# Kernel tuning notes

Hardware: AMD Instinct MI355X
Metric: run time of the kernel (lower is better)

Reference implementation:

```python
import jax, jax.numpy as jnp
from jax import lax
import numpy as np

B, T, H, V, C = 64, 64, 1024, 32000, 10
Z, CD = 32, 8  # latent dim, cond embedding dim


def lstm_scan(x_tbh, h0, c0, Wih, Whh, bih, bhh):
    """PyTorch-convention LSTM over time. x_tbh: [T,B,H]; returns hs [T,B,H]."""
    def step(carry, x):
        h, c = carry
        gates = x @ Wih.T + bih + h @ Whh.T + bhh  # [B,4H]
        i, f, g, o = jnp.split(gates, 4, axis=-1)
        c = jax.nn.sigmoid(f) * c + jax.nn.sigmoid(i) * jnp.tanh(g)
        h = jax.nn.sigmoid(o) * jnp.tanh(c)
        return (h, c), h
    _, hs = lax.scan(step, (h0, c0), x_tbh)
    return hs


def setup_inputs() -> dict:
    key = jax.random.key(0)
    ks = jax.random.split(key, 24)
    s = 0.02
    d = {
        'input_word': jax.random.randint(ks[0], (B, T), 0, V),
        'cond': jax.random.randint(ks[1], (B,), 0, C),
        'emb_N': jax.random.normal(ks[2], (V, H), jnp.float32) * s,
        'Wih_N': jax.random.normal(ks[3], (4 * H, H), jnp.float32) * s,
        'Whh_N': jax.random.normal(ks[4], (4 * H, H), jnp.float32) * s,
        'bih_N': jnp.zeros((4 * H,), jnp.float32),
        'bhh_N': jnp.zeros((4 * H,), jnp.float32),
        'emb_D': jax.random.normal(ks[5], (V, H), jnp.float32) * s,
        'Wih_D': jax.random.normal(ks[6], (4 * H, H), jnp.float32) * s,
        'Whh_D': jax.random.normal(ks[7], (4 * H, H), jnp.float32) * s,
        'bih_D': jnp.zeros((4 * H,), jnp.float32),
        'bhh_D': jnp.zeros((4 * H,), jnp.float32),
        'emb_cond': jax.random.normal(ks[8], (C, CD), jnp.float32) * s,
        'W_mean': jax.random.normal(ks[9], (Z, H), jnp.float32) * s,
        'b_mean': jnp.zeros((Z,), jnp.float32),
        'W_logvar': jax.random.normal(ks[10], (Z, H), jnp.float32) * s,
        'b_logvar': jnp.zeros((Z,), jnp.float32),
        'W_st': jax.random.normal(ks[11], (H, Z + CD), jnp.float32) * s,
        'b_st': jnp.zeros((H,), jnp.float32),
        'W_out': jax.random.normal(ks[12], (V, H), jnp.float32) * s,
        'b_out': jnp.zeros((V,), jnp.float32),
        'eps': jax.random.normal(ks[13], (B, Z), jnp.float32),
    }
    return d


def reference(input_word, cond, emb_N, Wih_N, Whh_N, bih_N, bhh_N,
              emb_D, Wih_D, Whh_D, bih_D, bhh_D, emb_cond,
              W_mean, b_mean, W_logvar, b_logvar, W_st, b_st,
              W_out, b_out, eps):
    cond_e = emb_cond[cond]                              # [B,8]
    # ---- encoder ----
    x_enc = jnp.transpose(emb_N[input_word], (1, 0, 2))  # [T,B,H]
    h0 = jnp.concatenate([jnp.zeros((B, H - CD), x_enc.dtype), cond_e], axis=-1)
    c0 = jnp.zeros((B, H), x_enc.dtype)
    hs = lstm_scan(x_enc, h0, c0, Wih_N, Whh_N, bih_N, bhh_N)
    h_t = hs[-1]                                         # [B,H]
    mean_h = h_t @ W_mean.T + b_mean                     # [B,32]
    logvar_h = h_t @ W_logvar.T + b_logvar               # [B,32]
    latent_h = eps * jnp.exp(0.5 * logvar_h) + mean_h    # reparameterize
    # ---- decoder (teacher forcing, start token 0) ----
    hd0 = jnp.concatenate([latent_h, cond_e], axis=-1) @ W_st.T + b_st  # [B,H]
    cd0 = jnp.zeros((B, H), hd0.dtype)
    dec_tok = jnp.concatenate(
        [jnp.zeros((B, 1), input_word.dtype), input_word[:, :-1]], axis=1)
    x_dec = jnp.transpose(emb_D[dec_tok], (1, 0, 2))     # [T,B,H]
    hs_d = lstm_scan(x_dec, hd0, cd0, Wih_D, Whh_D, bih_D, bhh_D)  # [T,B,H]
    logits = hs_d @ W_out.T + b_out                      # [T,B,V]
    return jnp.transpose(logits, (1, 0, 2))              # [B,T,V]
```

## Files before the change

kernel.cpp:

```cpp
#include <hip/hip_runtime.h>
#include <hip/hip_bf16.h>

typedef unsigned short u16;
typedef unsigned int   u32;
typedef unsigned long long u64;
typedef __attribute__((ext_vector_type(8))) short short8;
typedef __attribute__((ext_vector_type(4))) float f32x4;

#define DEVINL static __device__ __forceinline__

DEVINL u16 f2bf(float x) {
  u32 u = __float_as_uint(x);
  u32 r = (u + 0x7fffu + ((u >> 16) & 1u)) >> 16;
  return (u16)r;
}

#define GLD16(gp, lp) __builtin_amdgcn_global_load_lds(                     \
    (const __attribute__((address_space(1))) u32*)(gp),                     \
    (__attribute__((address_space(3))) u32*)(lp), 16, 0, 0)

__global__ __launch_bounds__(256) void conv_all(
    const float* __restrict__ s0, u16* __restrict__ d0,
    const float* __restrict__ s1, u16* __restrict__ d1,
    const float* __restrict__ s2, u16* __restrict__ d2,
    const float* __restrict__ s3, u16* __restrict__ d3,
    const float* __restrict__ s4, u16* __restrict__ d4) {
  const float* s; u16* d; int local;
  int blk = blockIdx.x;
  if (blk < 16384) {
    int p = blk >> 12; local = blk & 4095;
    s = (p == 0) ? s0 : (p == 1) ? s1 : (p == 2) ? s2 : s3;
    d = (p == 0) ? d0 : (p == 1) ? d1 : (p == 2) ? d2 : d3;
  } else {
    s = s4; d = d4; local = blk - 16384;
  }
  int i = local * 256 + threadIdx.x;
  float4 v = ((const float4*)s)[i];
  ushort4 o;
  o.x = f2bf(v.x); o.y = f2bf(v.y); o.z = f2bf(v.z); o.w = f2bf(v.w);
  ((ushort4*)d)[i] = o;
}

__global__ __launch_bounds__(256) void prep_small(
    const int* __restrict__ cond, const float* __restrict__ emb_cond,
    const float* __restrict__ bihN, const float* __restrict__ bhhN,
    const float* __restrict__ bihD, const float* __restrict__ bhhD,
    float* __restrict__ ce, float* __restrict__ biasN, float* __restrict__ biasD,
    u32* __restrict__ bar) {
  int tid = blockIdx.x * 256 + threadIdx.x;
  if (tid < 512) {
    int b = tid >> 3, j = tid & 7;
    ce[tid] = emb_cond[cond[b] * 8 + j];
  }
  int i = tid - 512;
  if (i >= 0 && i < 4096) {
    biasN[i] = bihN[i] + bhhN[i];
    biasD[i] = bihD[i] + bhhD[i];
  }
  int k = tid - 4608;
  if (k >= 0 && k < 512) bar[k] = 0;
}

__global__ __launch_bounds__(256) void init_enc(const float* __restrict__ ce,
                                                u16* __restrict__ hb0) {
  int tid = blockIdx.x * 256 + threadIdx.x;
  int b = tid >> 10, col = tid & 1023;
  float v = (col >= 1016) ? ce[b * 8 + (col - 1016)] : 0.f;
  hb0[tid] = f2bf(v);
}

__global__ __launch_bounds__(256) void gather_kernel(const float* __restrict__ emb,
                                                     const int* __restrict__ words,
                                                     u16* __restrict__ X, int dec) {
  int r = blockIdx.x;
  int t = r >> 6, b = r & 63;
  int tok = dec ? ((t == 0) ? 0 : words[b * 64 + t - 1]) : words[b * 64 + t];
  float4 v = ((const float4*)(emb + (size_t)tok * 1024))[threadIdx.x];
  ushort4 o;
  o.x = f2bf(v.x); o.y = f2bf(v.y); o.z = f2bf(v.z); o.w = f2bf(v.w);
  ((ushort4*)(X + (size_t)r * 1024))[threadIdx.x] = o;
}

DEVINL void gemm0_body(char* smemc, int bid, int nwg,
                       const u16* __restrict__ A, const u16* __restrict__ B,
                       float* __restrict__ C, const float* __restrict__ bias,
                       int N, int K) {
  u16 (*lA)[256 * 32] = (u16(*)[256 * 32])smemc;
  u16 (*lB)[128 * 32] = (u16(*)[128 * 32])(smemc + 32768);
  const int tid = threadIdx.x;
  const int lane = tid & 63;
  const int wid = tid >> 6;

  const int nn = N >> 7;
  const int wgid = (bid & 7) * (nwg >> 3) + (bid >> 3);
  const int tile_m = (wgid / nn) * 256;
  const int tile_n = (wgid % nn) * 128;
  const int wm = wid >> 1, wn = wid & 1;

  const int ldr = lane >> 2;
  const int lko = (lane & 3) * 8;
  const int l15 = lane & 15;
  const int g4 = lane >> 4;

  const size_t aBase = (size_t)tile_m * K;
  const size_t bBase = (size_t)tile_n * K;

  auto stage = [&](int buf, int k0) {
#pragma unroll
    for (int q = 0; q < 2; ++q) {
      int chk = wid * 2 + q;
      int row = chk * 16 + ldr;
      GLD16(A + aBase + (size_t)row * K + k0 + lko, &lA[buf][chk * 512]);
    }
    int row = wid * 16 + ldr;
    GLD16(B + bBase + (size_t)row * K + k0 + lko, &lB[buf][wid * 512]);
  };

  f32x4 acc[4][4];
#pragma unroll
  for (int i = 0; i < 4; ++i)
#pragma unroll
    for (int j = 0; j < 4; ++j) acc[i][j] = (f32x4)0.f;

  stage(0, 0);
  __syncthreads();

  const int NIT = K >> 5;
  for (int it = 0; it < NIT; ++it) {
    const int cur = it & 1;
    if (it + 1 < NIT) stage(cur ^ 1, (it + 1) * 32);
    short8 af[4], bf[4];
#pragma unroll
    for (int i = 0; i < 4; ++i)
      af[i] = *(const short8*)&lA[cur][(wm * 64 + i * 16 + l15) * 32 + g4 * 8];
#pragma unroll
    for (int j = 0; j < 4; ++j)
      bf[j] = *(const short8*)&lB[cur][(wn * 64 + j * 16 + l15) * 32 + g4 * 8];
#pragma unroll
    for (int i = 0; i < 4; ++i)
#pragma unroll
      for (int j = 0; j < 4; ++j)
        acc[i][j] = __builtin_amdgcn_mfma_f32_16x16x32_bf16(af[i], bf[j], acc[i][j], 0, 0, 0);
    __syncthreads();
  }

#pragma unroll
  for (int i = 0; i < 4; ++i) {
    int row0 = tile_m + wm * 64 + i * 16 + (g4 << 2);
#pragma unroll
    for (int j = 0; j < 4; ++j) {
      int col = tile_n + wn * 64 + j * 16 + l15;
      float bv = bias[col];
#pragma unroll
      for (int e = 0; e < 4; ++e)
        C[(size_t)(row0 + e) * (size_t)N + col] = acc[i][j][e] + bv;
    }
  }
}

DEVINL void lstm_body(char* smemc, const u16* __restrict__ Whh,
                      const float* __restrict__ Xp, u16* __restrict__ hbuf,
                      u16* __restrict__ hs_out, float* __restrict__ hT_out,
                      u32* arrive, int wgi) {
  char* smemA = smemc;
  float (*lg)[16][16] = (float(*)[16][16])(smemc + 32768);
  const int tid = threadIdx.x;
  const int lane = tid & 63;
  const int v = tid >> 6;
  const int gate = v >> 1;
  const int ch = v & 1;
  const int c = wgi >> 5;
  const int j = wgi & 31;
  const int b0 = c * 16, col0 = j * 32;
  const int l15 = lane & 15, g4 = lane >> 4;

  short8 breg[32];
  {
    const u16* Brow = Whh + (size_t)(gate * 1024 + col0 + ch * 16 + l15) * 1024
                          + g4 * 8;
#pragma unroll
    for (int kk = 0; kk < 32; ++kk)
      breg[kk] = *(const short8*)(Brow + kk * 32);
  }

  const int crow = tid >> 5, colw = tid & 31;
  const int bg = b0 + crow, cgl = col0 + colw;
  const int ch2 = colw >> 4, cw = colw & 15;
  float creg = 0.f;

  float xg0, xg1, xg2, xg3;
  {
    size_t xrow = (size_t)bg * 4096 + cgl;
    xg0 = __builtin_nontemporal_load(&Xp[xrow]);
    xg1 = __builtin_nontemporal_load(&Xp[xrow + 1024]);
    xg2 = __builtin_nontemporal_load(&Xp[xrow + 2048]);
    xg3 = __builtin_nontemporal_load(&Xp[xrow + 3072]);
  }

  for (int t = 0; t < 64; ++t) {
    const char* rbase = (const char*)(hbuf + (size_t)(t & 1) * 65536)
                      + (size_t)b0 * 2048;
    u32* wb32 = (u32*)(hbuf + (size_t)((t + 1) & 1) * 65536);

#pragma unroll
    for (int q = 0; q < 4; ++q) {
      int g = q * 512 + tid;
      int row = g >> 7;
      int cb = (g & 127) * 16;
      const u64* src = (const u64*)(rbase + (size_t)row * 2048 + cb);
      u64 lo = __hip_atomic_load(src,     __ATOMIC_RELAXED, __HIP_MEMORY_SCOPE_AGENT);
      u64 hi = __hip_atomic_load(src + 1, __ATOMIC_RELAXED, __HIP_MEMORY_SCOPE_AGENT);
      u64* d = (u64*)(smemA + row * 2048 + (cb ^ ((row & 7) << 4)));
      d[0] = lo; d[1] = hi;
    }
    __syncthreads();

    f32x4 a4[4] = {(f32x4)0.f, (f32x4)0.f, (f32x4)0.f, (f32x4)0.f};
#pragma unroll
    for (int kk = 0; kk < 32; ++kk) {
      int cb2 = kk * 64 + g4 * 16;
      const short8 a = *(const short8*)(smemA + l15 * 2048 + (cb2 ^ ((l15 & 7) << 4)));
      a4[kk & 3] = __builtin_amdgcn_mfma_f32_16x16x32_bf16(a, breg[kk], a4[kk & 3], 0, 0, 0);
    }
    f32x4 asum = a4[0] + a4[1] + a4[2] + a4[3];
    {
      int m = g4 * 4;
#pragma unroll
      for (int e = 0; e < 4; ++e) lg[v][m + e][l15] = asum[e];
    }
    __syncthreads();

    {
      float gi = lg[0 + ch2][crow][cw] + xg0;
      float gf = lg[2 + ch2][crow][cw] + xg1;
      float gg = lg[4 + ch2][crow][cw] + xg2;
      float go = lg[6 + ch2][crow][cw] + xg3;
      float si = 1.f / (1.f + __expf(-gi));
      float sf = 1.f / (1.f + __expf(-gf));
      float so = 1.f / (1.f + __expf(-go));
      float tg = tanhf(gg);
      float cn = sf * creg + si * tg;
      float hn = so * tanhf(cn);
      creg = cn;
      u16 h16 = f2bf(hn);
      u32 mine = h16;
      u32 other = (u32)__shfl_xor((int)mine, 1);
      if (!(colw & 1)) {
        u32 pk = mine | (other << 16);
        __hip_atomic_store(wb32 + (((size_t)bg * 1024 + cgl) >> 1), pk,
                           __ATOMIC_RELAXED, __HIP_MEMORY_SCOPE_AGENT);
      }
      if (hs_out) hs_out[((size_t)bg * 64 + t) * 1024 + cgl] = h16;
      if (hT_out && t == 63) hT_out[bg * 1024 + cgl] = hn;
    }

    if (t != 63) {
      {
        size_t xrow = (size_t)((t + 1) * 64 + bg) * 4096 + cgl;
        xg0 = __builtin_nontemporal_load(&Xp[xrow]);
        xg1 = __builtin_nontemporal_load(&Xp[xrow + 1024]);
        xg2 = __builtin_nontemporal_load(&Xp[xrow + 2048]);
        xg3 = __builtin_nontemporal_load(&Xp[xrow + 3072]);
      }
      u32 want = (u32)(t + 1);
      asm volatile("s_waitcnt vmcnt(0)" ::: "memory");
      __syncthreads();
      if (tid == 0)
        __hip_atomic_store(&arrive[wgi], want, __ATOMIC_RELAXED,
                           __HIP_MEMORY_SCOPE_AGENT);
      if (tid < 32) {
        int guard = 0;
        while (__hip_atomic_load(&arrive[c * 32 + tid], __ATOMIC_RELAXED,
                                 __HIP_MEMORY_SCOPE_AGENT) < want) {
          __builtin_amdgcn_s_sleep(2);
          if (++guard > (1 << 20)) break;
        }
      }
      __syncthreads();
    }
  }
}

__global__ __launch_bounds__(512, 1) void lstm_cluster(
    const u16* __restrict__ Whh, const float* __restrict__ Xp,
    u16* __restrict__ hbuf, u16* __restrict__ hs_out,
    float* __restrict__ hT_out, u32* arrive) {
  __shared__ __align__(16) char smem[40960];
  lstm_body(smem, Whh, Xp, hbuf, hs_out, hT_out, arrive, blockIdx.x);
}

__global__ __launch_bounds__(512) void gemm_bt0(
    const u16* __restrict__ A, const u16* __restrict__ B,
    float* __restrict__ C, const float* __restrict__ bias, int N, int K) {
  __shared__ __align__(16) char smem[49152];
  gemm0_body(smem, blockIdx.x, gridDim.x, A, B, C, bias, N, K);
}

__global__ __launch_bounds__(512, 1) void enc_fused(
    const u16* __restrict__ whhN, const float* __restrict__ XpE,
    u16* __restrict__ hbuf, float* __restrict__ hT_out, u32* arrive,
    const u16* __restrict__ Xd, const u16* __restrict__ wihD,
    float* __restrict__ XpD, const float* __restrict__ biasD) {
  __shared__ __align__(16) char smem[49152];
  if (blockIdx.x < 128)
    lstm_body(smem, whhN, XpE, hbuf, nullptr, hT_out, arrive, blockIdx.x);
  else
    gemm0_body(smem, blockIdx.x - 128, 512, Xd, wihD, XpD, biasD, 4096, 1024);
}

__global__ __launch_bounds__(512) void gemm_bt1(
    const u16* __restrict__ A, const u16* __restrict__ B,
    float* __restrict__ C, const float* __restrict__ bias, int N, int K) {
  __shared__ u16 lA[2][256 * 32];
  __shared__ u16 lB[2][128 * 32];
  const int tid = threadIdx.x;
  const int lane = tid & 63;
  const int wid = tid >> 6;

  const int i = blockIdx.x;
  const int x = i & 7;
  const int k = i >> 3;
  const int mg = k >> 6;
  const int r  = k & 63;
  const int kn = r >> 1;
  const int mi = r & 1;
  const int tn = kn * 8 + x;
  if (tn >= 250) return;
  const int tile_m = (mg * 2 + mi) * 256;
  const int tile_n = tn * 128;
  const int wm = wid >> 1, wn = wid & 1;

  const int ldr = lane >> 2;
  const int lko = (lane & 3) * 8;
  const int l15 = lane & 15;
  const int g4 = lane >> 4;

  const size_t aBase = (size_t)tile_m * K;
  const size_t bBase = (size_t)tile_n * K;

  auto stage = [&](int buf, int k0) {
#pragma unroll
    for (int q = 0; q < 2; ++q) {
      int chk = wid * 2 + q;
      int row = chk * 16 + ldr;
      GLD16(A + aBase + (size_t)row * K + k0 + lko, &lA[buf][chk * 512]);
    }
    int row = wid * 16 + ldr;
    GLD16(B + bBase + (size_t)row * K + k0 + lko, &lB[buf][wid * 512]);
  };

  f32x4 acc[4][4];
#pragma unroll
  for (int i2 = 0; i2 < 4; ++i2)
#pragma unroll
    for (int j2 = 0; j2 < 4; ++j2) acc[i2][j2] = (f32x4)0.f;

  stage(0, 0);
  __syncthreads();

  const int NIT = K >> 5;
  for (int it = 0; it < NIT; ++it) {
    const int cur = it & 1;
    if (it + 1 < NIT) stage(cur ^ 1, (it + 1) * 32);
    short8 af[4], bf[4];
#pragma unroll
    for (int i2 = 0; i2 < 4; ++i2)
      af[i2] = *(const short8*)&lA[cur][(wm * 64 + i2 * 16 + l15) * 32 + g4 * 8];
#pragma unroll
    for (int j2 = 0; j2 < 4; ++j2)
      bf[j2] = *(const short8*)&lB[cur][(wn * 64 + j2 * 16 + l15) * 32 + g4 * 8];
#pragma unroll
    for (int i2 = 0; i2 < 4; ++i2)
#pragma unroll
      for (int j2 = 0; j2 < 4; ++j2)
        acc[i2][j2] = __builtin_amdgcn_mfma_f32_16x16x32_bf16(af[i2], bf[j2], acc[i2][j2], 0, 0, 0);
    __syncthreads();
  }

#pragma unroll
  for (int i2 = 0; i2 < 4; ++i2) {
    int row0 = tile_m + wm * 64 + i2 * 16 + (g4 << 2);
#pragma unroll
    for (int j2 = 0; j2 < 4; ++j2) {
      int col = tile_n + wn * 64 + j2 * 16 + l15;
      float bv = bias[col];
#pragma unroll
      for (int e = 0; e < 4; ++e) {
        size_t o = (size_t)(row0 + e) * (size_t)N + col;
        __builtin_nontemporal_store(acc[i2][j2][e] + bv, &C[o]);
      }
    }
  }
}

__global__ __launch_bounds__(256) void latent_hd0_kernel(
    const float* hT, const float* Wm, const float* bm,
    const float* Wl, const float* bl, const float* Wst, const float* bst,
    const float* eps, const float* ce, u16* hb0) {
  __shared__ float red[64][4];
  __shared__ float ml[64];
  __shared__ float lat[40];
  int b = blockIdx.x;
  int tid = threadIdx.x;
  int o = tid >> 2, p = tid & 3;
  const float* w = (o < 32) ? (Wm + (size_t)o * 1024) : (Wl + (size_t)(o - 32) * 1024);
  const float* h = hT + (size_t)b * 1024;
  float s = 0.f;
  for (int k = p * 256; k < p * 256 + 256; ++k) s += h[k] * w[k];
  red[o][p] = s;
  __syncthreads();
  if (tid < 64) {
    float v = red[tid][0] + red[tid][1] + red[tid][2] + red[tid][3];
    v += (tid < 32) ? bm[tid] : bl[tid - 32];
    ml[tid] = v;
  }
  __syncthreads();
  if (tid < 32) lat[tid] = eps[b * 32 + tid] * __expf(0.5f * ml[32 + tid]) + ml[tid];
  if (tid >= 32 && tid < 40) lat[tid] = ce[b * 8 + (tid - 32)];
  __syncthreads();
  for (int hc = tid; hc < 1024; hc += 256) {
    float s2 = bst[hc];
    const float* wr = Wst + (size_t)hc * 40;
#pragma unroll
    for (int j = 0; j < 40; ++j) s2 += lat[j] * wr[j];
    hb0[b * 1024 + hc] = f2bf(s2);
  }
}

extern "C" void kernel_launch(void* const* d_in, const int* in_sizes, int n_in,
                              void* d_out, int out_size, void* d_ws, size_t ws_size,
                              hipStream_t stream) {
  const int*   input_word = (const int*)d_in[0];
  const int*   cond       = (const int*)d_in[1];
  const float* emb_N      = (const float*)d_in[2];
  const float* Wih_N      = (const float*)d_in[3];
  const float* Whh_N      = (const float*)d_in[4];
  const float* bih_N      = (const float*)d_in[5];
  const float* bhh_N      = (const float*)d_in[6];
  const float* emb_D      = (const float*)d_in[7];
  const float* Wih_D      = (const float*)d_in[8];
  const float* Whh_D      = (const float*)d_in[9];
  const float* bih_D      = (const float*)d_in[10];
  const float* bhh_D      = (const float*)d_in[11];
  const float* emb_cond   = (const float*)d_in[12];
  const float* W_mean     = (const float*)d_in[13];
  const float* b_mean     = (const float*)d_in[14];
  const float* W_logvar   = (const float*)d_in[15];
  const float* b_logvar   = (const float*)d_in[16];
  const float* W_st       = (const float*)d_in[17];
  const float* b_st       = (const float*)d_in[18];
  const float* W_out      = (const float*)d_in[19];
  const float* b_out      = (const float*)d_in[20];
  const float* eps        = (const float*)d_in[21];
  float* out = (float*)d_out;

  char* ws = (char*)d_ws;
  size_t off = 0;
  auto alloc = [&](size_t b) { size_t p = off; off += (b + 255) & ~(size_t)255; return p; };
  u16*   wihN = (u16*)(ws + alloc(4096ull * 1024 * 2));
  u16*   whhN = (u16*)(ws + alloc(4096ull * 1024 * 2));
  u16*   wihD = (u16*)(ws + alloc(4096ull * 1024 * 2));
  u16*   whhD = (u16*)(ws + alloc(4096ull * 1024 * 2));
  u16*   wout = (u16*)(ws + alloc(32000ull * 1024 * 2));
  u16*   Xe   = (u16*)(ws + alloc(4096ull * 1024 * 2));
  u16*   Xd   = (u16*)(ws + alloc(4096ull * 1024 * 2));
  float* Xp   = (float*)(ws + alloc(4096ull * 4096 * 4));
  u16*   hsd  = (u16*)(ws + alloc(4096ull * 1024 * 2));
  u16*   hb   = (u16*)(ws + alloc(2ull * 64 * 1024 * 2));
  float* hf   = (float*)(ws + alloc(64ull * 1024 * 4));
  float* biasN = (float*)(ws + alloc(4096 * 4));
  float* biasD = (float*)(ws + alloc(4096 * 4));
  float* ce    = (float*)(ws + alloc(64 * 8 * 4));
  u32*   bar   = (u32*)(ws + alloc(2048));
  size_t base_off = off;
  float* XpD2 = (float*)(ws + alloc(4096ull * 4096 * 4));
  if (base_off > ws_size) return;
  const bool fused = (off <= ws_size);
  float* XpD = fused ? XpD2 : Xp;

  conv_all<<<48384, 256, 0, stream>>>(Wih_N, wihN, Whh_N, whhN,
                                      Wih_D, wihD, Whh_D, whhD, W_out, wout);
  prep_small<<<20, 256, 0, stream>>>(cond, emb_cond, bih_N, bhh_N, bih_D, bhh_D,
                                     ce, biasN, biasD, bar);
  gather_kernel<<<4096, 256, 0, stream>>>(emb_N, input_word, Xe, 0);
  gather_kernel<<<4096, 256, 0, stream>>>(emb_D, input_word, Xd, 1);
  init_enc<<<256, 256, 0, stream>>>(ce, hb);

  gemm_bt0<<<512, 512, 0, stream>>>(Xe, wihN, Xp, biasN, 4096, 1024);
  if (fused) {
    enc_fused<<<640, 512, 0, stream>>>(whhN, Xp, hb, hf, bar + 0,
                                       Xd, wihD, XpD, biasD);
  } else {
    lstm_cluster<<<128, 512, 0, stream>>>(whhN, Xp, hb, nullptr, hf, bar + 0);
  }
  latent_hd0_kernel<<<64, 256, 0, stream>>>(hf, W_mean, b_mean, W_logvar, b_logvar,
                                            W_st, b_st, eps, ce, hb);
  if (!fused)
    gemm_bt0<<<512, 512, 0, stream>>>(Xd, wihD, XpD, biasD, 4096, 1024);
  lstm_cluster<<<128, 512, 0, stream>>>(whhD, XpD, hb, hsd, nullptr, bar + 256);
  gemm_bt1<<<4096, 512, 0, stream>>>(hsd, wout, out, b_out, 32000, 1024);
}
```

Measured before the change: 1.011 ms.

## Overlap output projection with decoder LSTM and fold W_out conversion into encoder

Merges the decoder LSTM and the vocab projection GEMM into one launch. The LSTM blocks publish per-cluster progress counters, and the GEMM blocks spin on these counters until the timesteps their tile needs have been written, so the logits GEMM can start before the recurrence finishes. hs is now stored time-major and the output index is remapped to keep the [B,T,V] layout. The W_out fp32→bf16 conversion moves out of the upfront conversion kernel into spare blocks of the fused encoder launch, where it overlaps the serial encoder LSTM. This relies on GEMM blocks that spin while the LSTM blocks are co-resident and still able to make progress, and on inter-block flag ordering, so it risks deadlock or stale reads.

After: 998.2 us. About the same (-1.3%).

```diff
diff --git a/kernel.cpp b/kernel.cpp
--- a/kernel.cpp
+++ b/kernel.cpp
@@ -19,22 +19,25 @@
     (const __attribute__((address_space(1))) u32*)(gp),                     \
     (__attribute__((address_space(3))) u32*)(lp), 16, 0, 0)
 
-__global__ __launch_bounds__(256) void conv_all(
+__global__ __launch_bounds__(256) void conv4(
     const float* __restrict__ s0, u16* __restrict__ d0,
     const float* __restrict__ s1, u16* __restrict__ d1,
     const float* __restrict__ s2, u16* __restrict__ d2,
-    const float* __restrict__ s3, u16* __restrict__ d3,
-    const float* __restrict__ s4, u16* __restrict__ d4) {
-  const float* s; u16* d; int local;
+    const float* __restrict__ s3, u16* __restrict__ d3) {
   int blk = blockIdx.x;
-  if (blk < 16384) {
-    int p = blk >> 12; local = blk & 4095;
-    s = (p == 0) ? s0 : (p == 1) ? s1 : (p == 2) ? s2 : s3;
-    d = (p == 0) ? d0 : (p == 1) ? d1 : (p == 2) ? d2 : d3;
-  } else {
-    s = s4; d = d4; local = blk - 16384;
-  }
+  int p = blk >> 12, local = blk & 4095;
+  const float* s = (p == 0) ? s0 : (p == 1) ? s1 : (p == 2) ? s2 : s3;
+  u16*         d = (p == 0) ? d0 : (p == 1) ? d1 : (p == 2) ? d2 : d3;
   int i = local * 256 + threadIdx.x;
+  float4 v = ((const float4*)s)[i];
+  ushort4 o;
+  o.x = f2bf(v.x); o.y = f2bf(v.y); o.z = f2bf(v.z); o.w = f2bf(v.w);
+  ((ushort4*)d)[i] = o;
+}
+
+__global__ __launch_bounds__(256) void conv_wout(const float* __restrict__ s,
+                                                 u16* __restrict__ d) {
+  int i = blockIdx.x * 256 + threadIdx.x;
   float4 v = ((const float4*)s)[i];
   ushort4 o;
   o.x = f2bf(v.x); o.y = f2bf(v.y); o.z = f2bf(v.z); o.w = f2bf(v.w);
@@ -58,7 +61,7 @@
     biasD[i] = bihD[i] + bhhD[i];
   }
   int k = tid - 4608;
-  if (k >= 0 && k < 512) bar[k] = 0;
+  if (k >= 0 && k < 1024) bar[k] = 0;
 }
 
 __global__ __launch_bounds__(256) void init_enc(const float* __restrict__ ce,
@@ -161,7 +164,7 @@
 DEVINL void lstm_body(char* smemc, const u16* __restrict__ Whh,
                       const float* __restrict__ Xp, u16* __restrict__ hbuf,
                       u16* __restrict__ hs_out, float* __restrict__ hT_out,
-                      u32* arrive, int wgi) {
+                      u32* arrive, u32* prog, int wgi) {
   char* smemA = smemc;
   float (*lg)[16][16] = (float(*)[16][16])(smemc + 32768);
   const int tid = threadIdx.x;
@@ -249,8 +252,10 @@
         u32 pk = mine | (other << 16);
         __hip_atomic_store(wb32 + (((size_t)bg * 1024 + cgl) >> 1), pk,
                            __ATOMIC_RELAXED, __HIP_MEMORY_SCOPE_AGENT);
+        if (hs_out)
+          __hip_atomic_store((u32*)hs_out + ((((size_t)t * 64 + bg) * 1024 + cgl) >> 1),
+                             pk, __ATOMIC_RELAXED, __HIP_MEMORY_SCOPE_AGENT);
       }
-      if (hs_out) hs_out[((size_t)bg * 64 + t) * 1024 + cgl] = h16;
       if (hT_out && t == 63) hT_out[bg * 1024 + cgl] = hn;
     }
 
@@ -277,16 +282,40 @@
         }
       }
       __syncthreads();
+      if (prog && j == 0 && tid == 0)
+        __hip_atomic_store(&prog[c], want, __ATOMIC_RELAXED,
+                           __HIP_MEMORY_SCOPE_AGENT);
+    }
+  }
+
+  if (prog) {
+    asm volatile("s_waitcnt vmcnt(0)" ::: "memory");
+    __syncthreads();
+    if (tid == 0)
+      __hip_atomic_store(&arrive[wgi], 64u, __ATOMIC_RELAXED,
+                         __HIP_MEMORY_SCOPE_AGENT);
+    if (j == 0) {
+      if (tid < 32) {
+        int guard = 0;
+        while (__hip_atomic_load(&arrive[c * 32 + tid], __ATOMIC_RELAXED,
+                                 __HIP_MEMORY_SCOPE_AGENT) < 64u) {
+          __builtin_amdgcn_s_sleep(2);
+          if (++guard > (1 << 20)) break;
+        }
+      }
+      __syncthreads();
+      if (tid == 0)
+        __hip_atomic_store(&prog[c], 64u, __ATOMIC_RELAXED,
+                           __HIP_MEMORY_SCOPE_AGENT);
     }
   }
 }
 
 __global__ __launch_bounds__(512, 1) void lstm_cluster(
     const u16* __restrict__ Whh, const float* __restrict__ Xp,
-    u16* __restrict__ hbuf, u16* __restrict__ hs_out,
-    float* __restrict__ hT_out, u32* arrive) {
+    u16* __restrict__ hbuf, float* __restrict__ hT_out, u32* arrive) {
   __shared__ __align__(16) char smem[40960];
-  lstm_body(smem, Whh, Xp, hbuf, hs_out, hT_out, arrive, blockIdx.x);
+  lstm_body(smem, Whh, Xp, hbuf, nullptr, hT_out, arrive, nullptr, blockIdx.x);
 }
 
 __global__ __launch_bounds__(512) void gemm_bt0(
@@ -300,24 +329,41 @@
     const u16* __restrict__ whhN, const float* __restrict__ XpE,
     u16* __restrict__ hbuf, float* __restrict__ hT_out, u32* arrive,
     const u16* __restrict__ Xd, const u16* __restrict__ wihD,
-    float* __restrict__ XpD, const float* __restrict__ biasD) {
+    float* __restrict__ XpD, const float* __restrict__ biasD,
+    const float* __restrict__ Wout, u16* __restrict__ wout) {
   __shared__ __align__(16) char smem[49152];
-  if (blockIdx.x < 128)
-    lstm_body(smem, whhN, XpE, hbuf, nullptr, hT_out, arrive, blockIdx.x);
-  else
+  if (blockIdx.x < 128) {
+    lstm_body(smem, whhN, XpE, hbuf, nullptr, hT_out, arrive, nullptr, blockIdx.x);
+  } else if (blockIdx.x < 640) {
     gemm0_body(smem, blockIdx.x - 128, 512, Xd, wihD, XpD, biasD, 4096, 1024);
-}
-
-__global__ __launch_bounds__(512) void gemm_bt1(
-    const u16* __restrict__ A, const u16* __restrict__ B,
-    float* __restrict__ C, const float* __restrict__ bias, int N, int K) {
-  __shared__ u16 lA[2][256 * 32];
-  __shared__ u16 lB[2][128 * 32];
+  } else {
+    int tid0 = (blockIdx.x - 640) * 512 + threadIdx.x;
+    for (int i = tid0; i < 8192000; i += 512 * 512) {
+      float4 v = ((const float4*)Wout)[i];
+      ushort4 o;
+      o.x = f2bf(v.x); o.y = f2bf(v.y); o.z = f2bf(v.z); o.w = f2bf(v.w);
+      ((ushort4*)wout)[i] = o;
+    }
+  }
+}
+
+__global__ __launch_bounds__(512, 1) void dec_fused(
+    const u16* __restrict__ whhD, const float* __restrict__ XpD,
+    u16* __restrict__ hbuf, u16* __restrict__ hsd, u32* arrive, u32* prog,
+    const u16* __restrict__ wout, float* __restrict__ out,
+    const float* __restrict__ b_out) {
+  __shared__ __align__(16) char smem[49152];
+  if (blockIdx.x < 128) {
+    lstm_body(smem, whhD, XpD, hbuf, hsd, nullptr, arrive, prog, blockIdx.x);
+    return;
+  }
+  u16 (*lA)[256 * 32] = (u16(*)[256 * 32])smem;
+  u16 (*lB)[128 * 32] = (u16(*)[128 * 32])(smem + 32768);
   const int tid = threadIdx.x;
   const int lane = tid & 63;
   const int wid = tid >> 6;
 
-  const int i = blockIdx.x;
+  const int i = blockIdx.x - 128;
   const int x = i & 7;
   const int k = i >> 3;
   const int mg = k >> 6;
@@ -326,9 +372,24 @@
   const int mi = r & 1;
   const int tn = kn * 8 + x;
   if (tn >= 250) return;
-  const int tile_m = (mg * 2 + mi) * 256;
+  const int mt = mg * 2 + mi;
+  const int tile_m = mt * 256;
   const int tile_n = tn * 128;
   const int wm = wid >> 1, wn = wid & 1;
+  const int N = 32000, K = 1024;
+
+  {
+    u32 need = (u32)(mt * 4 + 4);
+    if (tid < 4) {
+      int guard = 0;
+      while (__hip_atomic_load(&prog[tid], __ATOMIC_RELAXED,
+                               __HIP_MEMORY_SCOPE_AGENT) < need) {
+        __builtin_amdgcn_s_sleep(8);
+        if (++guard > (1 << 22)) break;
+      }
+    }
+    __syncthreads();
+  }
 
   const int ldr = lane >> 2;
   const int lko = (lane & 3) * 8;
@@ -338,30 +399,30 @@
   const size_t aBase = (size_t)tile_m * K;
   const size_t bBase = (size_t)tile_n * K;
 
-  auto stage = [&](int buf, int k0) {
+  f32x4 acc[4][4];
+#pragma unroll
+  for (int i2 = 0; i2 < 4; ++i2)
+#pragma unroll
+    for (int j2 = 0; j2 < 4; ++j2) acc[i2][j2] = (f32x4)0.f;
+
+  auto stg = [&](int buf, int k0) {
 #pragma unroll
     for (int q = 0; q < 2; ++q) {
       int chk = wid * 2 + q;
       int row = chk * 16 + ldr;
-      GLD16(A + aBase + (size_t)row * K + k0 + lko, &lA[buf][chk * 512]);
+      GLD16(hsd + aBase + (size_t)row * K + k0 + lko, &lA[buf][chk * 512]);
     }
     int row = wid * 16 + ldr;
-    GLD16(B + bBase + (size_t)row * K + k0 + lko, &lB[buf][wid * 512]);
+    GLD16(wout + bBase + (size_t)row * K + k0 + lko, &lB[buf][wid * 512]);
   };
 
-  f32x4 acc[4][4];
-#pragma unroll
-  for (int i2 = 0; i2 < 4; ++i2)
-#pragma unroll
-    for (int j2 = 0; j2 < 4; ++j2) acc[i2][j2] = (f32x4)0.f;
-
-  stage(0, 0);
+  stg(0, 0);
   __syncthreads();
 
   const int NIT = K >> 5;
   for (int it = 0; it < NIT; ++it) {
     const int cur = it & 1;
-    if (it + 1 < NIT) stage(cur ^ 1, (it + 1) * 32);
+    if (it + 1 < NIT) stg(cur ^ 1, (it + 1) * 32);
     short8 af[4], bf[4];
 #pragma unroll
     for (int i2 = 0; i2 < 4; ++i2)
@@ -383,11 +444,12 @@
 #pragma unroll
     for (int j2 = 0; j2 < 4; ++j2) {
       int col = tile_n + wn * 64 + j2 * 16 + l15;
-      float bv = bias[col];
+      float bv = b_out[col];
 #pragma unroll
       for (int e = 0; e < 4; ++e) {
-        size_t o = (size_t)(row0 + e) * (size_t)N + col;
-        __builtin_nontemporal_store(acc[i2][j2][e] + bv, &C[o]);
+        int rr = row0 + e;
+        size_t o = (size_t)((rr & 63) * 64 + (rr >> 6)) * (size_t)N + col;
+        __builtin_nontemporal_store(acc[i2][j2][e] + bv, &out[o]);
       }
     }
   }
@@ -471,16 +533,16 @@
   float* biasN = (float*)(ws + alloc(4096 * 4));
   float* biasD = (float*)(ws + alloc(4096 * 4));
   float* ce    = (float*)(ws + alloc(64 * 8 * 4));
-  u32*   bar   = (u32*)(ws + alloc(2048));
+  u32*   bar   = (u32*)(ws + alloc(4096));
   size_t base_off = off;
   float* XpD2 = (float*)(ws + alloc(4096ull * 4096 * 4));
   if (base_off > ws_size) return;
   const bool fused = (off <= ws_size);
   float* XpD = fused ? XpD2 : Xp;
 
-  conv_all<<<48384, 256, 0, stream>>>(Wih_N, wihN, Whh_N, whhN,
-                                      Wih_D, wihD, Whh_D, whhD, W_out, wout);
-  prep_small<<<20, 256, 0, stream>>>(cond, emb_cond, bih_N, bhh_N, bih_D, bhh_D,
+  conv4<<<16384, 256, 0, stream>>>(Wih_N, wihN, Whh_N, whhN,
+                                   Wih_D, wihD, Whh_D, whhD);
+  prep_small<<<22, 256, 0, stream>>>(cond, emb_cond, bih_N, bhh_N, bih_D, bhh_D,
                                      ce, biasN, biasD, bar);
   gather_kernel<<<4096, 256, 0, stream>>>(emb_N, input_word, Xe, 0);
   gather_kernel<<<4096, 256, 0, stream>>>(emb_D, input_word, Xd, 1);
@@ -488,15 +550,16 @@
 
   gemm_bt0<<<512, 512, 0, stream>>>(Xe, wihN, Xp, biasN, 4096, 1024);
   if (fused) {
-    enc_fused<<<640, 512, 0, stream>>>(whhN, Xp, hb, hf, bar + 0,
-                                       Xd, wihD, XpD, biasD);
+    enc_fused<<<1152, 512, 0, stream>>>(whhN, Xp, hb, hf, bar + 0,
+                                        Xd, wihD, XpD, biasD, W_out, wout);
   } else {
-    lstm_cluster<<<128, 512, 0, stream>>>(whhN, Xp, hb, nullptr, hf, bar + 0);
+    conv_wout<<<32000, 256, 0, stream>>>(W_out, wout);
+    lstm_cluster<<<128, 512, 0, stream>>>(whhN, Xp, hb, hf, bar + 0);
   }
   latent_hd0_kernel<<<64, 256, 0, stream>>>(hf, W_mean, b_mean, W_logvar, b_logvar,
                                             W_st, b_st, eps, ce, hb);
   if (!fused)
     gemm_bt0<<<512, 512, 0, stream>>>(Xd, wihD, XpD, biasD, 4096, 1024);
-  lstm_cluster<<<128, 512, 0, stream>>>(whhD, XpD, hb, hsd, nullptr, bar + 256);
-  gemm_bt1<<<4096, 512, 0, stream>>>(hsd, wout, out, b_out, 32000, 1024);
-}
+  dec_fused<<<4224, 512, 0, stream>>>(whhD, XpD, hb, hsd, bar + 256, bar + 512,
+                                      wout, out, b_out);
+}
```
